# Kernel optimization log

Hardware: AMD Instinct MI355X
Metric: run time of the kernel (lower is better)

The kernel has to match this reference:

```python
import jax, jax.numpy as jnp
import numpy as np

NUM_DIM = 3
WINDOW = 7
C = 96
H = 3
HEAD_DIM = C // H
SCALE = HEAD_DIM ** (-0.5)
N_WIN = 256
V = WINDOW ** NUM_DIM  # 343
TABLE = (2 * WINDOW - 1) ** NUM_DIM  # 2197


def _relative_position_index(dims):
    coords = np.stack(np.meshgrid(*[np.arange(d) for d in dims], indexing='ij'))
    coords = coords.reshape(len(dims), -1)  # (D, V)
    rel = coords[:, :, None] - coords[:, None, :]  # (D, V, V)
    rel = rel.transpose(1, 2, 0).copy()  # (V, V, D)
    for i, d in enumerate(dims):
        rel[:, :, i] += d - 1
    s = 1
    for i, d in enumerate(reversed(dims), 1):
        rel[:, :, -i] *= s
        s *= 2 * d - 1
    return rel.sum(-1)  # (V, V)


def setup_inputs() -> dict:
    key = jax.random.key(0)
    k1, k2, k3 = jax.random.split(key, 3)
    x = jax.random.normal(k1, (N_WIN, V, C), dtype=jnp.float32)
    mask = jnp.zeros((N_WIN, V, V), dtype=jnp.float32)
    w_qkv = jax.random.normal(k2, (3 * C, C), dtype=jnp.float32) * 0.02
    bias_table = jax.random.normal(k3, (H, TABLE), dtype=jnp.float32) * 0.02
    rel_index = jnp.asarray(_relative_position_index([WINDOW] * NUM_DIM), dtype=jnp.int32)
    return {"x": x, "mask": mask, "w_qkv": w_qkv, "bias_table": bias_table, "rel_index": rel_index}


def reference(x, mask, w_qkv, bias_table, rel_index):
    n, v, c = x.shape
    qkv = x @ w_qkv.T  # (N, V, 3C)
    qkv = qkv.reshape(n, v, 3, H, HEAD_DIM).transpose(2, 0, 3, 1, 4)  # (3, N, H, V, hd)
    q, k, vv = qkv[0], qkv[1], qkv[2]
    q = q * SCALE
    p = jnp.einsum('nhvc,nhuc->nhvu', q, k)  # (N, H, V, V)
    p = p + bias_table[:, rel_index]  # gather -> (H, V, V), broadcast over N
    p = p + mask[:, None]  # (N, 1, V, V)
    a = jax.nn.softmax(p, axis=-1)
    out = jnp.einsum('nhvu,nhuc->nhvc', a, vv)  # (N, H, V, hd)
    return out.transpose(0, 2, 1, 3).reshape(n, v, c)
```

## Files before the change

kernel.cpp:

```cpp
#include <hip/hip_runtime.h>
#include <hip/hip_bf16.h>

#define NWIN 256
#define NV 343
#define NC 96
#define NH 3
#define NTABLE 2197
#define SCALE_Q 0.17677669529663687f

typedef __attribute__((ext_vector_type(8))) short bf16x8;
typedef __attribute__((ext_vector_type(4))) float f32x4;

static __device__ __forceinline__ unsigned short f2b(float f) {
    union { __hip_bfloat16 b; unsigned short u; } cv;
    cv.b = __float2bfloat16(f);
    return cv.u;
}
static __device__ __forceinline__ float b2f(unsigned short u) {
    union { unsigned short u; __hip_bfloat16 b; } cv;
    cv.u = u;
    return __bfloat162float(cv.b);
}
static __device__ __forceinline__ f32x4 mfma16(bf16x8 a, bf16x8 b, f32x4 c) {
    return __builtin_amdgcn_mfma_f32_16x16x32_bf16(a, b, c, 0, 0, 0);
}
static __device__ __forceinline__ bf16x8 ldx8(const float* p) {
    float4 x0 = *(const float4*)p;
    float4 x1 = *(const float4*)(p + 4);
    bf16x8 t;
    t[0] = (short)f2b(x0.x); t[1] = (short)f2b(x0.y);
    t[2] = (short)f2b(x0.z); t[3] = (short)f2b(x0.w);
    t[4] = (short)f2b(x1.x); t[5] = (short)f2b(x1.y);
    t[6] = (short)f2b(x1.z); t[7] = (short)f2b(x1.w);
    return t;
}

#define WS_NEEDED (288 * 96 * 2)

__global__ __launch_bounds__(256) void wcvt(const float* __restrict__ w,
                                            unsigned short* __restrict__ wbf) {
    int i = blockIdx.x * 256 + threadIdx.x;
    float v = w[i];
    if (i < 96 * 96) v *= SCALE_Q;
    wbf[i] = f2b(v);
}

#define AK_K   0
#define AK_V   22528
#define AK_B   45056
#define AK_MC  49456
#define AK_QP  50144
#define AK_LDS 54240

__global__ __launch_bounds__(256, 3) void attn(
    const float* __restrict__ x, const float* __restrict__ mask,
    const unsigned short* __restrict__ wbf, const float* __restrict__ bias_table,
    float* __restrict__ out)
{
    __shared__ char lds[AK_LDS];
    unsigned short* bias_l = (unsigned short*)(lds + AK_B);
    short* mcode = (short*)(lds + AK_MC);

    const int tid = threadIdx.x;
    const int lane = tid & 63;
    const int wvv = tid >> 6;
    const int l15 = lane & 15;
    const int l4 = lane >> 4;

    int bid = blockIdx.x;
    int linear = (bid & 7) * 96 + (bid >> 3);
    int n = linear / 3;
    int h = linear - n * 3;

    for (int i = tid; i < NTABLE; i += 256) bias_l[i] = f2b(bias_table[h * NTABLE + i]);
    for (int i = tid; i < NV; i += 256) {
        int cz = i / 49; int rr = i - cz * 49; int cy = rr / 7; int cx = rr - cy * 7;
        mcode[i] = (short)(cz * 169 + cy * 13 + cx);
    }

    const unsigned short* wqp = wbf + (h * 32) * NC;
    const unsigned short* wkp = wbf + (96 + h * 32) * NC;
    const unsigned short* wvp = wbf + (192 + h * 32) * NC;
    const float* xn = x + (size_t)n * NV * NC;

#define BFRAG(WP, T, KS) (*(const bf16x8*)((WP) + ((T) * 16 + l15) * NC + (KS) * 32 + l4 * 8))

    #pragma unroll 1
    for (int mc = 0; mc < 6; ++mc) {
        int r0 = mc * 64 + wvv * 16;
        if (r0 >= 352) continue;
        int rr = min(r0 + l15, NV - 1);
        const float* xp = xn + (size_t)rr * NC + l4 * 8;
        bf16x8 a0 = ldx8(xp), a1 = ldx8(xp + 32), a2 = ldx8(xp + 64);
        f32x4 k0 = {0.f,0.f,0.f,0.f}, k1 = {0.f,0.f,0.f,0.f};
        f32x4 v0 = {0.f,0.f,0.f,0.f}, v1 = {0.f,0.f,0.f,0.f};
        k0 = mfma16(a0, BFRAG(wkp,0,0), k0); k0 = mfma16(a1, BFRAG(wkp,0,1), k0); k0 = mfma16(a2, BFRAG(wkp,0,2), k0);
        k1 = mfma16(a0, BFRAG(wkp,1,0), k1); k1 = mfma16(a1, BFRAG(wkp,1,1), k1); k1 = mfma16(a2, BFRAG(wkp,1,2), k1);
        v0 = mfma16(a0, BFRAG(wvp,0,0), v0); v0 = mfma16(a1, BFRAG(wvp,0,1), v0); v0 = mfma16(a2, BFRAG(wvp,0,2), v0);
        v1 = mfma16(a0, BFRAG(wvp,1,0), v1); v1 = mfma16(a1, BFRAG(wvp,1,1), v1); v1 = mfma16(a2, BFRAG(wvp,1,2), v1);
        int t0 = r0 + l4 * 4;
        #pragma unroll
        for (int j = 0; j < 4; ++j) {
            int row = t0 + j;
            int sw = (row & 3) << 4;
            *(unsigned short*)(lds + AK_K + ((row * 64 + l15 * 2) ^ sw)) = f2b(k0[j]);
            *(unsigned short*)(lds + AK_K + ((row * 64 + 32 + l15 * 2) ^ sw)) = f2b(k1[j]);
        }
        {
            int vsw = (l15 & 3) << 4;
            ushort4 pk;
            pk.x = f2b(v0[0]); pk.y = f2b(v0[1]); pk.z = f2b(v0[2]); pk.w = f2b(v0[3]);
            *(ushort4*)(lds + AK_V + ((l15 * 704 + t0 * 2) ^ vsw)) = pk;
            ushort4 pk2;
            pk2.x = f2b(v1[0]); pk2.y = f2b(v1[1]); pk2.z = f2b(v1[2]); pk2.w = f2b(v1[3]);
            *(ushort4*)(lds + AK_V + (((16 + l15) * 704 + t0 * 2) ^ vsw)) = pk2;
        }
    }
    __syncthreads();

    const float* maskn = mask + (size_t)n * NV * NV;

    #pragma unroll 1
    for (int mc = 0; mc < 6; ++mc) {
        int r0 = mc * 64 + wvv * 16;
        if (r0 >= 352) continue;
        int t0 = r0 + l4 * 4;

        {
            int rr = min(r0 + l15, NV - 1);
            const float* xp = xn + (size_t)rr * NC + l4 * 8;
            bf16x8 a0 = ldx8(xp), a1 = ldx8(xp + 32), a2 = ldx8(xp + 64);
            f32x4 q0 = {0.f,0.f,0.f,0.f}, q1 = {0.f,0.f,0.f,0.f};
            q0 = mfma16(a0, BFRAG(wqp,0,0), q0); q0 = mfma16(a1, BFRAG(wqp,0,1), q0); q0 = mfma16(a2, BFRAG(wqp,0,2), q0);
            q1 = mfma16(a0, BFRAG(wqp,1,0), q1); q1 = mfma16(a1, BFRAG(wqp,1,1), q1); q1 = mfma16(a2, BFRAG(wqp,1,2), q1);
            #pragma unroll
            for (int j = 0; j < 4; ++j) {
                int row = wvv * 16 + l4 * 4 + j;
                int sw = (row & 3) << 4;
                *(unsigned short*)(lds + AK_QP + ((row * 64 + l15 * 2) ^ sw)) = f2b(q0[j]);
                *(unsigned short*)(lds + AK_QP + ((row * 64 + 32 + l15 * 2) ^ sw)) = f2b(q1[j]);
            }
        }
        asm volatile("s_waitcnt lgkmcnt(0)" ::: "memory");
        __builtin_amdgcn_sched_barrier(0);
        const int qrow = wvv * 16 + l15;
        const int paaddr = AK_QP + ((qrow * 64 + l4 * 16) ^ ((qrow & 3) << 4));
        bf16x8 qa = *(const bf16x8*)(lds + paaddr);

        float m0 = -1e30f, m1 = -1e30f, m2 = -1e30f, m3 = -1e30f;
        float L0 = 0.f, L1 = 0.f, L2 = 0.f, L3 = 0.f;
        f32x4 o0 = {0.f,0.f,0.f,0.f}, o1 = {0.f,0.f,0.f,0.f};
        int mv0 = (int)mcode[min(t0 + 0, NV - 1)] + 1098;
        int mv1 = (int)mcode[min(t0 + 1, NV - 1)] + 1098;
        int mv2 = (int)mcode[min(t0 + 2, NV - 1)] + 1098;
        int mv3 = (int)mcode[min(t0 + 3, NV - 1)] + 1098;
        const float* mrow0 = maskn + (size_t)min(t0 + 0, NV - 1) * NV;
        const float* mrow1 = maskn + (size_t)min(t0 + 1, NV - 1) * NV;
        const float* mrow2 = maskn + (size_t)min(t0 + 2, NV - 1) * NV;
        const float* mrow3 = maskn + (size_t)min(t0 + 3, NV - 1) * NV;

        #pragma unroll
        for (int tt = 0; tt < 11; ++tt) {
            const int u0 = tt * 32 + l15;
            const int u1i = tt * 32 + 16 + l15;
            const int u1 = (tt == 10) ? min(u1i, NV - 1) : u1i;
            float mk00 = mrow0[u0], mk01 = mrow1[u0], mk02 = mrow2[u0], mk03 = mrow3[u0];
            float mk10 = mrow0[u1], mk11 = mrow1[u1], mk12 = mrow2[u1], mk13 = mrow3[u1];
            int krow0 = tt * 32 + l15;
            bf16x8 kb0 = *(const bf16x8*)(lds + AK_K + ((krow0 * 64 + l4 * 16) ^ ((krow0 & 3) << 4)));
            int krow1 = krow0 + 16;
            bf16x8 kb1 = *(const bf16x8*)(lds + AK_K + ((krow1 * 64 + l4 * 16) ^ ((krow1 & 3) << 4)));
            f32x4 z = {0.f,0.f,0.f,0.f};
            f32x4 p0 = mfma16(qa, kb0, z);
            f32x4 p1 = mfma16(qa, kb1, z);
            int mu0 = (int)mcode[u0];
            int mu1 = (int)mcode[u1];
            float v00 = p0[0] + b2f(bias_l[mv0 - mu0]) + mk00;
            float v01 = p0[1] + b2f(bias_l[mv1 - mu0]) + mk01;
            float v02 = p0[2] + b2f(bias_l[mv2 - mu0]) + mk02;
            float v03 = p0[3] + b2f(bias_l[mv3 - mu0]) + mk03;
            float v10 = p1[0] + b2f(bias_l[mv0 - mu1]) + mk10;
            float v11 = p1[1] + b2f(bias_l[mv1 - mu1]) + mk11;
            float v12 = p1[2] + b2f(bias_l[mv2 - mu1]) + mk12;
            float v13 = p1[3] + b2f(bias_l[mv3 - mu1]) + mk13;
            if (tt == 10) {
                bool ok = (l15 < 7);
                v10 = ok ? v10 : -1e30f; v11 = ok ? v11 : -1e30f;
                v12 = ok ? v12 : -1e30f; v13 = ok ? v13 : -1e30f;
            }
            float pm0 = fmaxf(v00, v10), pm1 = fmaxf(v01, v11);
            float pm2 = fmaxf(v02, v12), pm3 = fmaxf(v03, v13);
            #pragma unroll
            for (int mm = 1; mm < 16; mm <<= 1) {
                pm0 = fmaxf(pm0, __shfl_xor(pm0, mm, 64));
                pm1 = fmaxf(pm1, __shfl_xor(pm1, mm, 64));
                pm2 = fmaxf(pm2, __shfl_xor(pm2, mm, 64));
                pm3 = fmaxf(pm3, __shfl_xor(pm3, mm, 64));
            }
            float dmax = fmaxf(fmaxf(pm0 - m0, pm1 - m1), fmaxf(pm2 - m2, pm3 - m3));
            if (__any(dmax > 8.0f)) {
                float mn, sc;
                mn = fmaxf(m0, pm0); sc = __expf(m0 - mn); L0 *= sc; o0[0] *= sc; o1[0] *= sc; m0 = mn;
                mn = fmaxf(m1, pm1); sc = __expf(m1 - mn); L1 *= sc; o0[1] *= sc; o1[1] *= sc; m1 = mn;
                mn = fmaxf(m2, pm2); sc = __expf(m2 - mn); L2 *= sc; o0[2] *= sc; o1[2] *= sc; m2 = mn;
                mn = fmaxf(m3, pm3); sc = __expf(m3 - mn); L3 *= sc; o0[3] *= sc; o1[3] *= sc; m3 = mn;
            }
            float e00 = __expf(v00 - m0), e01 = __expf(v01 - m1);
            float e02 = __expf(v02 - m2), e03 = __expf(v03 - m3);
            float e10 = __expf(v10 - m0), e11 = __expf(v11 - m1);
            float e12 = __expf(v12 - m2), e13 = __expf(v13 - m3);
            L0 += e00 + e10; L1 += e01 + e11; L2 += e02 + e12; L3 += e03 + e13;
            {
                int pr = wvv * 16 + l4 * 4;
                int sw0 = ((pr + 0) & 3) << 4, sw1 = ((pr + 1) & 3) << 4;
                int sw2 = ((pr + 2) & 3) << 4, sw3 = ((pr + 3) & 3) << 4;
                *(unsigned short*)(lds + AK_QP + (((pr + 0) * 64 + l15 * 2) ^ sw0)) = f2b(e00);
                *(unsigned short*)(lds + AK_QP + (((pr + 1) * 64 + l15 * 2) ^ sw1)) = f2b(e01);
                *(unsigned short*)(lds + AK_QP + (((pr + 2) * 64 + l15 * 2) ^ sw2)) = f2b(e02);
                *(unsigned short*)(lds + AK_QP + (((pr + 3) * 64 + l15 * 2) ^ sw3)) = f2b(e03);
                *(unsigned short*)(lds + AK_QP + (((pr + 0) * 64 + 32 + l15 * 2) ^ sw0)) = f2b(e10);
                *(unsigned short*)(lds + AK_QP + (((pr + 1) * 64 + 32 + l15 * 2) ^ sw1)) = f2b(e11);
                *(unsigned short*)(lds + AK_QP + (((pr + 2) * 64 + 32 + l15 * 2) ^ sw2)) = f2b(e12);
                *(unsigned short*)(lds + AK_QP + (((pr + 3) * 64 + 32 + l15 * 2) ^ sw3)) = f2b(e13);
            }
            int vt0 = (tt * 32 + l4 * 8) * 2;
            int vswA = (l15 & 3) << 4;
            bf16x8 vb0 = *(const bf16x8*)(lds + AK_V + ((l15 * 704 + vt0) ^ vswA));
            bf16x8 vb1 = *(const bf16x8*)(lds + AK_V + (((16 + l15) * 704 + vt0) ^ vswA));
            asm volatile("s_waitcnt lgkmcnt(0)" ::: "memory");
            __builtin_amdgcn_sched_barrier(0);
            bf16x8 pa = *(const bf16x8*)(lds + paaddr);
            o0 = mfma16(pa, vb0, o0);
            o1 = mfma16(pa, vb1, o1);
        }

        #pragma unroll
        for (int mm = 1; mm < 16; mm <<= 1) {
            L0 += __shfl_xor(L0, mm, 64);
            L1 += __shfl_xor(L1, mm, 64);
            L2 += __shfl_xor(L2, mm, 64);
            L3 += __shfl_xor(L3, mm, 64);
        }
        float Ls[4] = {L0, L1, L2, L3};
        #pragma unroll
        for (int j = 0; j < 4; ++j) {
            int tok = t0 + j;
            if (tok < NV) {
                float inv = 1.0f / Ls[j];
                float* op = out + ((size_t)n * NV + tok) * NC + h * 32;
                op[l15] = o0[j] * inv;
                op[16 + l15] = o1[j] * inv;
            }
        }
    }
#undef BFRAG
}

#define OFF_Q    0
#define OFF_K    22528
#define OFF_VT   45056
#define OFF_BIAS 67584
#define OFF_MC   76384
#define OFF_U    77760
#define OFF_XS   OFF_U
#define OFF_WS   (OFF_U + 13312)
#define OFF_PS   OFF_U
#define LDS_BYTES (OFF_U + 45056)
#define VPAD 352

__global__ __launch_bounds__(256) void wattn(
    const float* __restrict__ x, const float* __restrict__ mask,
    const float* __restrict__ w_qkv, const float* __restrict__ bias_table,
    const int* __restrict__ rel_index, float* __restrict__ out)
{
    extern __shared__ char flds[];
    unsigned short* q_s  = (unsigned short*)(flds + OFF_Q);
    unsigned short* k_s  = (unsigned short*)(flds + OFF_K);
    unsigned short* v_t  = (unsigned short*)(flds + OFF_VT);
    float*          bias_l = (float*)(flds + OFF_BIAS);
    int*            mcode  = (int*)(flds + OFF_MC);
    unsigned short* xs   = (unsigned short*)(flds + OFF_XS);
    unsigned short* ws   = (unsigned short*)(flds + OFF_WS);
    unsigned short* p_s  = (unsigned short*)(flds + OFF_PS);

    const int tid = threadIdx.x;
    const int lane = tid & 63;
    const int wv  = tid >> 6;
    const int l15 = lane & 15;
    const int l4  = lane >> 4;

    int bid = blockIdx.x;
    int linear = (bid & 7) * 96 + (bid >> 3);
    int n = linear / 3;
    int h = linear - n * 3;

    for (int i = tid; i < NTABLE; i += 256) bias_l[i] = bias_table[h * NTABLE + i];
    for (int i = tid; i < NV; i += 256) {
        int cz = i / 49; int rr = i - cz * 49; int cy = rr / 7; int cx = rr - cy * 7;
        mcode[i] = cz * 169 + cy * 13 + cx;
    }
    for (int i = tid; i < 96 * 24; i += 256) {
        int nr = i / 24, c4 = i - nr * 24;
        int g = nr >> 5, d = nr & 31;
        const float4 wq = *(const float4*)(w_qkv + (size_t)(g * NC + h * 32 + d) * NC + c4 * 4);
        float s = (g == 0) ? SCALE_Q : 1.0f;
        unsigned short* dst = ws + nr * 104 + c4 * 4;
        dst[0] = f2b(wq.x * s); dst[1] = f2b(wq.y * s);
        dst[2] = f2b(wq.z * s); dst[3] = f2b(wq.w * s);
    }
    for (int mc = 0; mc < 6; ++mc) {
        __syncthreads();
        for (int i = tid; i < 64 * 24; i += 256) {
            int r = i / 24, c4 = i - r * 24;
            int tok = mc * 64 + r;
            float4 xv = make_float4(0.f, 0.f, 0.f, 0.f);
            if (tok < NV) xv = *(const float4*)(x + ((size_t)n * NV + tok) * NC + c4 * 4);
            unsigned short* dst = xs + r * 104 + c4 * 4;
            dst[0] = f2b(xv.x); dst[1] = f2b(xv.y); dst[2] = f2b(xv.z); dst[3] = f2b(xv.w);
        }
        __syncthreads();
        int r0 = mc * 64 + wv * 16;
        if (r0 < VPAD) {
            bf16x8 a[3];
            #pragma unroll
            for (int ks = 0; ks < 3; ++ks)
                a[ks] = *(const bf16x8*)(xs + (wv * 16 + l15) * 104 + ks * 32 + l4 * 8);
            #pragma unroll
            for (int nt = 0; nt < 6; ++nt) {
                f32x4 acc = {0.f, 0.f, 0.f, 0.f};
                #pragma unroll
                for (int ks = 0; ks < 3; ++ks) {
                    bf16x8 b = *(const bf16x8*)(ws + (nt * 16 + l15) * 104 + ks * 32 + l4 * 8);
                    acc = mfma16(a[ks], b, acc);
                }
                int ch = (nt & 1) * 16 + l15;
                int t0 = r0 + l4 * 4;
                if (nt < 2) {
                    #pragma unroll
                    for (int j = 0; j < 4; ++j) q_s[(t0 + j) * 32 + ch] = f2b(acc[j]);
                } else if (nt < 4) {
                    #pragma unroll
                    for (int j = 0; j < 4; ++j) k_s[(t0 + j) * 32 + ch] = f2b(acc[j]);
                } else {
                    ushort4 pk;
                    pk.x = f2b(acc[0]); pk.y = f2b(acc[1]);
                    pk.z = f2b(acc[2]); pk.w = f2b(acc[3]);
                    *(ushort4*)(v_t + ch * VPAD + t0) = pk;
                }
            }
        }
    }
    __syncthreads();

    const float* maskn = mask + (size_t)n * NV * NV;
    for (int mc = 0; mc < 6; ++mc) {
        int r0 = mc * 64 + wv * 16;
        if (r0 >= VPAD) continue;
        int t0 = r0 + l4 * 4;
        float mk[22][4];
        #pragma unroll
        for (int t = 0; t < 22; ++t) {
            int u = t * 16 + l15;
            #pragma unroll
            for (int j = 0; j < 4; ++j) {
                int tok = t0 + j;
                mk[t][j] = (u < NV && tok < NV) ? maskn[(size_t)tok * NV + u] : 0.f;
            }
        }
        bf16x8 qa = *(const bf16x8*)(q_s + (r0 + l15) * 32 + l4 * 8);
        f32x4 p[22];
        #pragma unroll
        for (int t = 0; t < 22; ++t) {
            bf16x8 kb = *(const bf16x8*)(k_s + (t * 16 + l15) * 32 + l4 * 8);
            f32x4 z = {0.f, 0.f, 0.f, 0.f};
            p[t] = mfma16(qa, kb, z);
        }
        int mv[4];
        #pragma unroll
        for (int j = 0; j < 4; ++j) {
            int tok = t0 + j;
            mv[j] = mcode[tok < NV ? tok : 0] + 1098;
        }
        float rmax[4] = {-1e30f, -1e30f, -1e30f, -1e30f};
        #pragma unroll
        for (int t = 0; t < 22; ++t) {
            int u = t * 16 + l15;
            bool uv = (u < NV);
            int mu = mcode[uv ? u : 0];
            #pragma unroll
            for (int j = 0; j < 4; ++j) {
                float val = p[t][j] + bias_l[mv[j] - mu] + mk[t][j];
                val = uv ? val : -1e30f;
                p[t][j] = val;
                rmax[j] = fmaxf(rmax[j], val);
            }
        }
        #pragma unroll
        for (int m = 1; m < 16; m <<= 1) {
            #pragma unroll
            for (int j = 0; j < 4; ++j)
                rmax[j] = fmaxf(rmax[j], __shfl_xor(rmax[j], m, 64));
        }
        float rsum[4] = {0.f, 0.f, 0.f, 0.f};
        #pragma unroll
        for (int t = 0; t < 22; ++t) {
            #pragma unroll
            for (int j = 0; j < 4; ++j) {
                float e = __expf(p[t][j] - rmax[j]);
                rsum[j] += e;
                p_s[(wv * 16 + l4 * 4 + j) * VPAD + t * 16 + l15] = f2b(e);
            }
        }
        #pragma unroll
        for (int m = 1; m < 16; m <<= 1) {
            #pragma unroll
            for (int j = 0; j < 4; ++j)
                rsum[j] += __shfl_xor(rsum[j], m, 64);
        }
        f32x4 o0 = {0.f,0.f,0.f,0.f}, o1 = {0.f,0.f,0.f,0.f};
        #pragma unroll
        for (int ks = 0; ks < 11; ++ks) {
            bf16x8 pa  = *(const bf16x8*)(p_s + (wv * 16 + l15) * VPAD + ks * 32 + l4 * 8);
            bf16x8 vb0 = *(const bf16x8*)(v_t + l15 * VPAD + ks * 32 + l4 * 8);
            bf16x8 vb1 = *(const bf16x8*)(v_t + (16 + l15) * VPAD + ks * 32 + l4 * 8);
            o0 = mfma16(pa, vb0, o0);
            o1 = mfma16(pa, vb1, o1);
        }
        #pragma unroll
        for (int j = 0; j < 4; ++j) {
            int tok = t0 + j;
            if (tok < NV) {
                float inv = 1.0f / rsum[j];
                float* op = out + ((size_t)n * NV + tok) * NC + h * 32;
                op[l15]      = o0[j] * inv;
                op[16 + l15] = o1[j] * inv;
            }
        }
    }
}

extern "C" void kernel_launch(void* const* d_in, const int* in_sizes, int n_in,
                              void* d_out, int out_size, void* d_ws, size_t ws_size,
                              hipStream_t stream) {
    const float* x          = (const float*)d_in[0];
    const float* mask       = (const float*)d_in[1];
    const float* w_qkv      = (const float*)d_in[2];
    const float* bias_table = (const float*)d_in[3];
    const int*   rel_index  = (const int*)d_in[4];
    float* out = (float*)d_out;

    (void)rel_index; (void)in_sizes; (void)n_in; (void)out_size;

    if (ws_size >= WS_NEEDED) {
        unsigned short* wbf = (unsigned short*)d_ws;
        wcvt<<<dim3(108), dim3(256), 0, stream>>>(w_qkv, wbf);
        attn<<<dim3(NWIN * NH), dim3(256), 0, stream>>>(x, mask, wbf, bias_table, out);
    } else {
        hipFuncSetAttribute((const void*)wattn, hipFuncAttributeMaxDynamicSharedMemorySize, LDS_BYTES);
        wattn<<<dim3(NWIN * NH), dim3(256), LDS_BYTES, stream>>>(x, mask, w_qkv, bias_table, rel_index, out);
    }
}
```

Baseline: 344.9 us.

## Keep softmax probabilities in registers via transposed scores and drop online max

```diff
diff --git a/kernel.cpp b/kernel.cpp
--- a/kernel.cpp
+++ b/kernel.cpp
@@ -7,6 +7,7 @@
 #define NH 3
 #define NTABLE 2197
 #define SCALE_Q 0.17677669529663687f
+#define LOG2E 1.4426950408889634f
 
 typedef __attribute__((ext_vector_type(8))) short bf16x8;
 typedef __attribute__((ext_vector_type(4))) float f32x4;
@@ -41,7 +42,7 @@
                                             unsigned short* __restrict__ wbf) {
     int i = blockIdx.x * 256 + threadIdx.x;
     float v = w[i];
-    if (i < 96 * 96) v *= SCALE_Q;
+    if (i < 96 * 96) v *= SCALE_Q * LOG2E;
     wbf[i] = f2b(v);
 }
 
@@ -49,8 +50,8 @@
 #define AK_V   22528
 #define AK_B   45056
 #define AK_MC  49456
-#define AK_QP  50144
-#define AK_LDS 54240
+#define AK_QP  50160
+#define AK_LDS 54256
 
 __global__ __launch_bounds__(256, 3) void attn(
     const float* __restrict__ x, const float* __restrict__ mask,
@@ -72,9 +73,11 @@
     int n = linear / 3;
     int h = linear - n * 3;
 
-    for (int i = tid; i < NTABLE; i += 256) bias_l[i] = f2b(bias_table[h * NTABLE + i]);
-    for (int i = tid; i < NV; i += 256) {
-        int cz = i / 49; int rr = i - cz * 49; int cy = rr / 7; int cx = rr - cy * 7;
+    for (int i = tid; i < NTABLE; i += 256)
+        bias_l[i] = f2b(bias_table[h * NTABLE + i] * LOG2E);
+    for (int i = tid; i < 352; i += 256) {
+        int t = min(i, NV - 1);
+        int cz = t / 49; int rr = t - cz * 49; int cy = rr / 7; int cx = rr - cy * 7;
         mcode[i] = (short)(cz * 169 + cy * 13 + cx);
     }
 
@@ -107,13 +110,16 @@
             *(unsigned short*)(lds + AK_K + ((row * 64 + 32 + l15 * 2) ^ sw)) = f2b(k1[j]);
         }
         {
+            int rb = t0 & 31;
+            int sbase = (rb < 16) ? ((rb >> 2) * 8) : ((((rb - 16) >> 2) * 8) + 4);
+            int colb = ((t0 >> 5) * 32 + sbase) * 2;
             int vsw = (l15 & 3) << 4;
             ushort4 pk;
             pk.x = f2b(v0[0]); pk.y = f2b(v0[1]); pk.z = f2b(v0[2]); pk.w = f2b(v0[3]);
-            *(ushort4*)(lds + AK_V + ((l15 * 704 + t0 * 2) ^ vsw)) = pk;
+            *(ushort4*)(lds + AK_V + ((l15 * 704 + colb) ^ vsw)) = pk;
             ushort4 pk2;
             pk2.x = f2b(v1[0]); pk2.y = f2b(v1[1]); pk2.z = f2b(v1[2]); pk2.w = f2b(v1[3]);
-            *(ushort4*)(lds + AK_V + (((16 + l15) * 704 + t0 * 2) ^ vsw)) = pk2;
+            *(ushort4*)(lds + AK_V + (((16 + l15) * 704 + colb) ^ vsw)) = pk2;
         }
     }
     __syncthreads();
@@ -144,111 +150,83 @@
         asm volatile("s_waitcnt lgkmcnt(0)" ::: "memory");
         __builtin_amdgcn_sched_barrier(0);
         const int qrow = wvv * 16 + l15;
-        const int paaddr = AK_QP + ((qrow * 64 + l4 * 16) ^ ((qrow & 3) << 4));
-        bf16x8 qa = *(const bf16x8*)(lds + paaddr);
-
-        float m0 = -1e30f, m1 = -1e30f, m2 = -1e30f, m3 = -1e30f;
-        float L0 = 0.f, L1 = 0.f, L2 = 0.f, L3 = 0.f;
+        bf16x8 qa = *(const bf16x8*)(lds + AK_QP + ((qrow * 64 + l4 * 16) ^ ((qrow & 3) << 4)));
+
+        const int qr = min(r0 + l15, NV - 1);
+        const float* mrow = maskn + (size_t)qr * NV;
+        const int mvq = (int)mcode[qr] + 1098;
+
+        float L = 0.f;
         f32x4 o0 = {0.f,0.f,0.f,0.f}, o1 = {0.f,0.f,0.f,0.f};
-        int mv0 = (int)mcode[min(t0 + 0, NV - 1)] + 1098;
-        int mv1 = (int)mcode[min(t0 + 1, NV - 1)] + 1098;
-        int mv2 = (int)mcode[min(t0 + 2, NV - 1)] + 1098;
-        int mv3 = (int)mcode[min(t0 + 3, NV - 1)] + 1098;
-        const float* mrow0 = maskn + (size_t)min(t0 + 0, NV - 1) * NV;
-        const float* mrow1 = maskn + (size_t)min(t0 + 1, NV - 1) * NV;
-        const float* mrow2 = maskn + (size_t)min(t0 + 2, NV - 1) * NV;
-        const float* mrow3 = maskn + (size_t)min(t0 + 3, NV - 1) * NV;
+
+        float mkc[8], mkn[8];
+        #pragma unroll
+        for (int j = 0; j < 4; ++j) {
+            mkc[j]     = mrow[l4 * 4 + j];
+            mkc[4 + j] = mrow[16 + l4 * 4 + j];
+        }
 
         #pragma unroll
         for (int tt = 0; tt < 11; ++tt) {
-            const int u0 = tt * 32 + l15;
-            const int u1i = tt * 32 + 16 + l15;
-            const int u1 = (tt == 10) ? min(u1i, NV - 1) : u1i;
-            float mk00 = mrow0[u0], mk01 = mrow1[u0], mk02 = mrow2[u0], mk03 = mrow3[u0];
-            float mk10 = mrow0[u1], mk11 = mrow1[u1], mk12 = mrow2[u1], mk13 = mrow3[u1];
             int krow0 = tt * 32 + l15;
             bf16x8 kb0 = *(const bf16x8*)(lds + AK_K + ((krow0 * 64 + l4 * 16) ^ ((krow0 & 3) << 4)));
             int krow1 = krow0 + 16;
             bf16x8 kb1 = *(const bf16x8*)(lds + AK_K + ((krow1 * 64 + l4 * 16) ^ ((krow1 & 3) << 4)));
             f32x4 z = {0.f,0.f,0.f,0.f};
-            f32x4 p0 = mfma16(qa, kb0, z);
-            f32x4 p1 = mfma16(qa, kb1, z);
-            int mu0 = (int)mcode[u0];
-            int mu1 = (int)mcode[u1];
-            float v00 = p0[0] + b2f(bias_l[mv0 - mu0]) + mk00;
-            float v01 = p0[1] + b2f(bias_l[mv1 - mu0]) + mk01;
-            float v02 = p0[2] + b2f(bias_l[mv2 - mu0]) + mk02;
-            float v03 = p0[3] + b2f(bias_l[mv3 - mu0]) + mk03;
-            float v10 = p1[0] + b2f(bias_l[mv0 - mu1]) + mk10;
-            float v11 = p1[1] + b2f(bias_l[mv1 - mu1]) + mk11;
-            float v12 = p1[2] + b2f(bias_l[mv2 - mu1]) + mk12;
-            float v13 = p1[3] + b2f(bias_l[mv3 - mu1]) + mk13;
-            if (tt == 10) {
-                bool ok = (l15 < 7);
-                v10 = ok ? v10 : -1e30f; v11 = ok ? v11 : -1e30f;
-                v12 = ok ? v12 : -1e30f; v13 = ok ? v13 : -1e30f;
-            }
-            float pm0 = fmaxf(v00, v10), pm1 = fmaxf(v01, v11);
-            float pm2 = fmaxf(v02, v12), pm3 = fmaxf(v03, v13);
-            #pragma unroll
-            for (int mm = 1; mm < 16; mm <<= 1) {
-                pm0 = fmaxf(pm0, __shfl_xor(pm0, mm, 64));
-                pm1 = fmaxf(pm1, __shfl_xor(pm1, mm, 64));
-                pm2 = fmaxf(pm2, __shfl_xor(pm2, mm, 64));
-                pm3 = fmaxf(pm3, __shfl_xor(pm3, mm, 64));
-            }
-            float dmax = fmaxf(fmaxf(pm0 - m0, pm1 - m1), fmaxf(pm2 - m2, pm3 - m3));
-            if (__any(dmax > 8.0f)) {
-                float mn, sc;
-                mn = fmaxf(m0, pm0); sc = __expf(m0 - mn); L0 *= sc; o0[0] *= sc; o1[0] *= sc; m0 = mn;
-                mn = fmaxf(m1, pm1); sc = __expf(m1 - mn); L1 *= sc; o0[1] *= sc; o1[1] *= sc; m1 = mn;
-                mn = fmaxf(m2, pm2); sc = __expf(m2 - mn); L2 *= sc; o0[2] *= sc; o1[2] *= sc; m2 = mn;
-                mn = fmaxf(m3, pm3); sc = __expf(m3 - mn); L3 *= sc; o0[3] *= sc; o1[3] *= sc; m3 = mn;
-            }
-            float e00 = __expf(v00 - m0), e01 = __expf(v01 - m1);
-            float e02 = __expf(v02 - m2), e03 = __expf(v03 - m3);
-            float e10 = __expf(v10 - m0), e11 = __expf(v11 - m1);
-            float e12 = __expf(v12 - m2), e13 = __expf(v13 - m3);
-            L0 += e00 + e10; L1 += e01 + e11; L2 += e02 + e12; L3 += e03 + e13;
-            {
-                int pr = wvv * 16 + l4 * 4;
-                int sw0 = ((pr + 0) & 3) << 4, sw1 = ((pr + 1) & 3) << 4;
-                int sw2 = ((pr + 2) & 3) << 4, sw3 = ((pr + 3) & 3) << 4;
-                *(unsigned short*)(lds + AK_QP + (((pr + 0) * 64 + l15 * 2) ^ sw0)) = f2b(e00);
-                *(unsigned short*)(lds + AK_QP + (((pr + 1) * 64 + l15 * 2) ^ sw1)) = f2b(e01);
-                *(unsigned short*)(lds + AK_QP + (((pr + 2) * 64 + l15 * 2) ^ sw2)) = f2b(e02);
-                *(unsigned short*)(lds + AK_QP + (((pr + 3) * 64 + l15 * 2) ^ sw3)) = f2b(e03);
-                *(unsigned short*)(lds + AK_QP + (((pr + 0) * 64 + 32 + l15 * 2) ^ sw0)) = f2b(e10);
-                *(unsigned short*)(lds + AK_QP + (((pr + 1) * 64 + 32 + l15 * 2) ^ sw1)) = f2b(e11);
-                *(unsigned short*)(lds + AK_QP + (((pr + 2) * 64 + 32 + l15 * 2) ^ sw2)) = f2b(e12);
-                *(unsigned short*)(lds + AK_QP + (((pr + 3) * 64 + 32 + l15 * 2) ^ sw3)) = f2b(e13);
-            }
-            int vt0 = (tt * 32 + l4 * 8) * 2;
-            int vswA = (l15 & 3) << 4;
-            bf16x8 vb0 = *(const bf16x8*)(lds + AK_V + ((l15 * 704 + vt0) ^ vswA));
-            bf16x8 vb1 = *(const bf16x8*)(lds + AK_V + (((16 + l15) * 704 + vt0) ^ vswA));
-            asm volatile("s_waitcnt lgkmcnt(0)" ::: "memory");
-            __builtin_amdgcn_sched_barrier(0);
-            bf16x8 pa = *(const bf16x8*)(lds + paaddr);
+            f32x4 st0 = mfma16(kb0, qa, z);
+            f32x4 st1 = mfma16(kb1, qa, z);
+
+            if (tt < 10) {
+                int ub = (tt + 1) * 32 + l4 * 4;
+                #pragma unroll
+                for (int j = 0; j < 4; ++j) {
+                    mkn[j]     = mrow[ub + j];
+                    mkn[4 + j] = mrow[min(ub + 16 + j, NV - 1)];
+                }
+            }
+
+            short4 mcA = *(const short4*)(mcode + tt * 32 + l4 * 4);
+            short4 mcB = *(const short4*)(mcode + tt * 32 + 16 + l4 * 4);
+            int muA[4] = {mcA.x, mcA.y, mcA.z, mcA.w};
+            int muB[4] = {mcB.x, mcB.y, mcB.z, mcB.w};
+
+            float e[8];
+            #pragma unroll
+            for (int j = 0; j < 4; ++j) {
+                float vA = st0[j] + b2f(bias_l[mvq - muA[j]]) + mkc[j] * LOG2E;
+                e[j] = exp2f(vA);
+                float vB = st1[j] + b2f(bias_l[mvq - muB[j]]) + mkc[4 + j] * LOG2E;
+                if (tt == 10) vB = (l4 * 4 + j < 7) ? vB : -1e30f;
+                e[4 + j] = exp2f(vB);
+            }
+            L += ((e[0] + e[1]) + (e[2] + e[3])) + ((e[4] + e[5]) + (e[6] + e[7]));
+
+            bf16x8 pa;
+            #pragma unroll
+            for (int i = 0; i < 8; ++i) pa[i] = (short)f2b(e[i]);
+
+            int vcol = (tt * 32 + l4 * 8) * 2;
+            int vsw = (l15 & 3) << 4;
+            bf16x8 vb0 = *(const bf16x8*)(lds + AK_V + ((l15 * 704 + vcol) ^ vsw));
+            bf16x8 vb1 = *(const bf16x8*)(lds + AK_V + (((16 + l15) * 704 + vcol) ^ vsw));
             o0 = mfma16(pa, vb0, o0);
             o1 = mfma16(pa, vb1, o1);
-        }
-
-        #pragma unroll
-        for (int mm = 1; mm < 16; mm <<= 1) {
-            L0 += __shfl_xor(L0, mm, 64);
-            L1 += __shfl_xor(L1, mm, 64);
-            L2 += __shfl_xor(L2, mm, 64);
-            L3 += __shfl_xor(L3, mm, 64);
-        }
-        float Ls[4] = {L0, L1, L2, L3};
+
+            #pragma unroll
+            for (int i = 0; i < 8; ++i) mkc[i] = mkn[i];
+        }
+
+        L += __shfl_xor(L, 16, 64);
+        L += __shfl_xor(L, 32, 64);
+
         #pragma unroll
         for (int j = 0; j < 4; ++j) {
+            float Lr = __shfl(L, l4 * 4 + j, 64);
             int tok = t0 + j;
             if (tok < NV) {
-                float inv = 1.0f / Ls[j];
+                float inv = 1.0f / Lr;
                 float* op = out + ((size_t)n * NV + tok) * NC + h * 32;
-                op[l15] = o0[j] * inv;
+                op[l15]      = o0[j] * inv;
                 op[16 + l15] = o1[j] * inv;
             }
         }
```

After: 287.5 us. 16.6% less time.
